# Kernel optimization log

Hardware: AMD Instinct MI355X
Metric: run time of the kernel (lower is better)

Reference implementation:

```python
import jax, jax.numpy as jnp
import numpy as np
import math

D_MODEL = 256
N_HEADS = 4
WINDOW = 5
LN_EPS = 1e-5


def setup_inputs() -> dict:
    key = jax.random.key(0)
    ks = jax.random.split(key, 10)
    B, S, D = 8, 8192, D_MODEL
    s = 1.0 / math.sqrt(D)
    x = jax.random.normal(ks[0], (B, S, D), dtype=jnp.float32)
    Wq = jax.random.uniform(ks[1], (D, D), jnp.float32, -s, s)
    bq = jax.random.uniform(ks[2], (D,), jnp.float32, -s, s)
    Wk = jax.random.uniform(ks[3], (D, D), jnp.float32, -s, s)
    bk = jax.random.uniform(ks[4], (D,), jnp.float32, -s, s)
    Wv = jax.random.uniform(ks[5], (D, D), jnp.float32, -s, s)
    bv = jax.random.uniform(ks[6], (D,), jnp.float32, -s, s)
    Wo = jax.random.uniform(ks[7], (D, D), jnp.float32, -s, s)
    bo = jax.random.uniform(ks[8], (D,), jnp.float32, -s, s)
    gamma = jnp.ones((D,), jnp.float32)
    beta = jnp.zeros((D,), jnp.float32)
    return {"x": x, "Wq": Wq, "bq": bq, "Wk": Wk, "bk": bk,
            "Wv": Wv, "bv": bv, "Wo": Wo, "bo": bo,
            "gamma": gamma, "beta": beta}


def _layer_norm(y, gamma, beta):
    mu = jnp.mean(y, axis=-1, keepdims=True)
    var = jnp.mean(jnp.square(y - mu), axis=-1, keepdims=True)
    return (y - mu) * jax.lax.rsqrt(var + LN_EPS) * gamma + beta


def reference(x, Wq, bq, Wk, bk, Wv, bv, Wo, bo, gamma, beta):
    B, S, D = x.shape
    H, hd, W = N_HEADS, D // N_HEADS, WINDOW
    num_windows = (S + W - 1) // W
    pad_len = num_windows * W - S
    Sp = S + pad_len

    def proj(Wm, bm):
        # (B,S,D) -> (B,H,S,hd)
        p = (x @ Wm.T + bm).reshape(B, S, H, hd).transpose(0, 2, 1, 3)
        if pad_len > 0:
            p = jnp.pad(p, ((0, 0), (0, 0), (0, pad_len), (0, 0)))
        return p.reshape(B, H, num_windows, W, hd)

    Q = proj(Wq, bq)
    K = proj(Wk, bk)
    V = proj(Wv, bv)

    scores = jnp.einsum('bhnwd,bhnvd->bhnwv', Q, K) / math.sqrt(hd)
    attn = jax.nn.softmax(scores, axis=-1)  # dropout is identity in eval
    out = jnp.tanh(jnp.einsum('bhnwv,bhnvd->bhnwd', attn, V))

    out = out.reshape(B, H, Sp, hd)[:, :, :S, :]
    out = out.transpose(0, 2, 1, 3).reshape(B, S, D)
    out = out @ Wo.T + bo
    return _layer_norm(out + x, gamma, beta)
```

## Files before the change

### kernel.cpp

```cpp
#include <hip/hip_runtime.h>
#include <hip/hip_bf16.h>
#include <stdint.h>

typedef unsigned short u16;
typedef __attribute__((ext_vector_type(8))) __bf16 bf16x8;
typedef __attribute__((ext_vector_type(4))) float f32x4;

#define DEV static __device__ __forceinline__

DEV u16 f32_to_bf16(float f) {
  uint32_t u = __float_as_uint(f);
  u += 0x7fffu + ((u >> 16) & 1u);
  return (u16)(u >> 16);
}

DEV void unpack8(uint4 u, float* f) {
  uint32_t a[4] = {u.x, u.y, u.z, u.w};
#pragma unroll
  for (int i = 0; i < 4; ++i) {
    f[2 * i]     = __uint_as_float(a[i] << 16);
    f[2 * i + 1] = __uint_as_float(a[i] & 0xffff0000u);
  }
}

DEV uint4 pack8(const float* f) {
  uint32_t a[4];
#pragma unroll
  for (int i = 0; i < 4; ++i)
    a[i] = (uint32_t)f32_to_bf16(f[2 * i]) | ((uint32_t)f32_to_bf16(f[2 * i + 1]) << 16);
  return make_uint4(a[0], a[1], a[2], a[3]);
}

__global__ __launch_bounds__(256) void convert_kernel(
    const float* __restrict__ x, const float* __restrict__ Wq,
    const float* __restrict__ Wk, const float* __restrict__ Wv,
    const float* __restrict__ Wo, u16* __restrict__ xb,
    u16* __restrict__ wqkv, u16* __restrict__ wob) {
  const size_t NX4 = (size_t)65536 * 256 / 4;
  size_t i = (size_t)blockIdx.x * 256 + threadIdx.x;
  const float* src;
  u16* dst;
  size_t off4;
  if (i < NX4) {
    src = x; dst = xb; off4 = i;
  } else {
    size_t w = i - NX4;
    int which = (int)(w >> 14);
    off4 = w & 16383;
    if (which == 0)      { src = Wq; dst = wqkv; }
    else if (which == 1) { src = Wk; dst = wqkv + 65536; }
    else if (which == 2) { src = Wv; dst = wqkv + 131072; }
    else                 { src = Wo; dst = wob; }
  }
  float4 v = reinterpret_cast<const float4*>(src)[off4];
  ushort4 o;
  o.x = f32_to_bf16(v.x); o.y = f32_to_bf16(v.y);
  o.z = f32_to_bf16(v.z); o.w = f32_to_bf16(v.w);
  reinterpret_cast<ushort4*>(dst)[off4] = o;
}

__global__ __launch_bounds__(256) void qkv_gemm(
    const u16* __restrict__ Xb, const u16* __restrict__ Wqkv,
    const float* __restrict__ bq, const float* __restrict__ bk,
    const float* __restrict__ bv, u16* __restrict__ QKV) {
  __shared__ u16 As[128][40];
  __shared__ u16 Bs[128][40];
  const int bn = blockIdx.x;
  const int bm = blockIdx.y;
  const int tid = threadIdx.x;
  const int lane = tid & 63;
  const int wid = tid >> 6;
  const int wm = (wid >> 1) * 64;
  const int wn = (wid & 1) * 64;
  const int fr = lane & 15;
  const int fq = lane >> 4;

  f32x4 acc[4][4] = {};

  const int tr = tid >> 1;
  const int tc = (tid & 1) << 4;
  const u16* Ag = Xb + (size_t)(bm * 128 + tr) * 256 + tc;
  const u16* Bg = Wqkv + (size_t)(bn * 128 + tr) * 256 + tc;

  for (int kt = 0; kt < 8; ++kt) {
    uint4 a0 = *reinterpret_cast<const uint4*>(Ag + kt * 32);
    uint4 a1 = *reinterpret_cast<const uint4*>(Ag + kt * 32 + 8);
    uint4 b0 = *reinterpret_cast<const uint4*>(Bg + kt * 32);
    uint4 b1 = *reinterpret_cast<const uint4*>(Bg + kt * 32 + 8);
    __syncthreads();
    *reinterpret_cast<uint4*>(&As[tr][tc]) = a0;
    *reinterpret_cast<uint4*>(&As[tr][tc + 8]) = a1;
    *reinterpret_cast<uint4*>(&Bs[tr][tc]) = b0;
    *reinterpret_cast<uint4*>(&Bs[tr][tc + 8]) = b1;
    __syncthreads();
    bf16x8 af[4], bf[4];
#pragma unroll
    for (int m = 0; m < 4; ++m)
      af[m] = *reinterpret_cast<const bf16x8*>(&As[wm + m * 16 + fr][fq * 8]);
#pragma unroll
    for (int n = 0; n < 4; ++n)
      bf[n] = *reinterpret_cast<const bf16x8*>(&Bs[wn + n * 16 + fr][fq * 8]);
#pragma unroll
    for (int m = 0; m < 4; ++m)
#pragma unroll
      for (int n = 0; n < 4; ++n)
        acc[m][n] = __builtin_amdgcn_mfma_f32_16x16x32_bf16(af[m], bf[n], acc[m][n], 0, 0, 0);
  }

  const float* bias = (bn < 2) ? (bq + (bn & 1) * 128)
                    : (bn < 4) ? (bk + ((bn - 2) & 1) * 128)
                               : (bv + ((bn - 4) & 1) * 128);
  float bv4[4];
#pragma unroll
  for (int n = 0; n < 4; ++n) bv4[n] = bias[wn + n * 16 + fr];

#pragma unroll
  for (int m = 0; m < 4; ++m) {
#pragma unroll
    for (int r = 0; r < 4; ++r) {
      int row = bm * 128 + wm + m * 16 + fq * 4 + r;
      u16* orow = QKV + (size_t)row * 768 + bn * 128;
#pragma unroll
      for (int n = 0; n < 4; ++n)
        orow[wn + n * 16 + fr] = f32_to_bf16(acc[m][n][r] + bv4[n]);
    }
  }
}

__global__ __launch_bounds__(256) void attn_kernel(const u16* __restrict__ QKV,
                                                   u16* __restrict__ AO) {
  const int S = 8192, NW = 1639, CH = 205;
  int wgid = blockIdx.x * 4 + (threadIdx.x >> 6);
  int lane = threadIdx.x & 63;
  int b = wgid / (4 * CH);
  int rm = wgid % (4 * CH);
  int h = rm / CH;
  int ch = rm % CH;
  int w = ch * 8 + (lane >> 3);
  int t = lane & 7;
  bool wv = (w < NW);

  float kv[5][8], vv[5][8];
#pragma unroll
  for (int j = 0; j < 5; ++j) {
    int s = w * 5 + j;
    if (wv && s < S) {
      size_t off = ((size_t)b * S + s) * 768 + h * 64 + t * 8;
      unpack8(*reinterpret_cast<const uint4*>(QKV + off + 256), kv[j]);
      unpack8(*reinterpret_cast<const uint4*>(QKV + off + 512), vv[j]);
    } else {
#pragma unroll
      for (int d = 0; d < 8; ++d) { kv[j][d] = 0.f; vv[j][d] = 0.f; }
    }
  }

#pragma unroll
  for (int i = 0; i < 5; ++i) {
    int s = w * 5 + i;
    bool sv = wv && (s < S);
    float q[8];
    if (sv) {
      size_t off = ((size_t)b * S + s) * 768 + h * 64 + t * 8;
      unpack8(*reinterpret_cast<const uint4*>(QKV + off), q);
    } else {
#pragma unroll
      for (int d = 0; d < 8; ++d) q[d] = 0.f;
    }
    float sc[5];
#pragma unroll
    for (int j = 0; j < 5; ++j) {
      float p = 0.f;
#pragma unroll
      for (int d = 0; d < 8; ++d) p += q[d] * kv[j][d];
      sc[j] = p;
    }
#pragma unroll
    for (int mask = 1; mask <= 4; mask <<= 1)
#pragma unroll
      for (int j = 0; j < 5; ++j) sc[j] += __shfl_xor(sc[j], mask);
#pragma unroll
    for (int j = 0; j < 5; ++j) sc[j] *= 0.125f;
    float mx = sc[0];
#pragma unroll
    for (int j = 1; j < 5; ++j) mx = fmaxf(mx, sc[j]);
    float e[5], sum = 0.f;
#pragma unroll
    for (int j = 0; j < 5; ++j) { e[j] = __expf(sc[j] - mx); sum += e[j]; }
    float inv = 1.0f / sum;
    float o[8];
#pragma unroll
    for (int d = 0; d < 8; ++d) {
      float a = 0.f;
#pragma unroll
      for (int j = 0; j < 5; ++j) a += e[j] * vv[j][d];
      float v2 = a * inv;
      float e2 = __expf(2.0f * v2);
      o[d] = 1.0f - 2.0f / (e2 + 1.0f);
    }
    if (sv) {
      size_t oo = ((size_t)b * S + s) * 256 + h * 64 + t * 8;
      *reinterpret_cast<uint4*>(AO + oo) = pack8(o);
    }
  }
}

__global__ __launch_bounds__(256) void o_gemm_ln(
    const u16* __restrict__ AO, const u16* __restrict__ Wob,
    const float* __restrict__ bo, const float* __restrict__ x,
    const float* __restrict__ gamma, const float* __restrict__ beta,
    float* __restrict__ out) {
  __shared__ u16 As[64][40];
  __shared__ u16 Bs[256][40];
  __shared__ float pS[4][64], pQ[4][64];
  __shared__ float muS[64], rsS[64];
  const int bm = blockIdx.x;
  const int tid = threadIdx.x;
  const int lane = tid & 63;
  const int wid = tid >> 6;
  const int wn = wid * 64;
  const int fr = lane & 15;
  const int fq = lane >> 4;

  f32x4 acc[4][4] = {};

  const int ar = tid >> 2;
  const int ac = (tid & 3) << 3;
  const u16* Ag = AO + (size_t)(bm * 64 + ar) * 256 + ac;

  for (int kt = 0; kt < 8; ++kt) {
    uint4 a = *reinterpret_cast<const uint4*>(Ag + kt * 32);
    uint4 bvv[4];
#pragma unroll
    for (int j = 0; j < 4; ++j)
      bvv[j] = *reinterpret_cast<const uint4*>(Wob + (size_t)(ar + j * 64) * 256 + kt * 32 + ac);
    __syncthreads();
    *reinterpret_cast<uint4*>(&As[ar][ac]) = a;
#pragma unroll
    for (int j = 0; j < 4; ++j)
      *reinterpret_cast<uint4*>(&Bs[ar + j * 64][ac]) = bvv[j];
    __syncthreads();
    bf16x8 af[4], bf[4];
#pragma unroll
    for (int m = 0; m < 4; ++m)
      af[m] = *reinterpret_cast<const bf16x8*>(&As[m * 16 + fr][fq * 8]);
#pragma unroll
    for (int n = 0; n < 4; ++n)
      bf[n] = *reinterpret_cast<const bf16x8*>(&Bs[wn + n * 16 + fr][fq * 8]);
#pragma unroll
    for (int m = 0; m < 4; ++m)
#pragma unroll
      for (int n = 0; n < 4; ++n)
        acc[m][n] = __builtin_amdgcn_mfma_f32_16x16x32_bf16(af[m], bf[n], acc[m][n], 0, 0, 0);
  }

  float bov[4], gv[4], bev[4];
#pragma unroll
  for (int n = 0; n < 4; ++n) {
    int c = wn + n * 16 + fr;
    bov[n] = bo[c]; gv[n] = gamma[c]; bev[n] = beta[c];
  }
#pragma unroll
  for (int m = 0; m < 4; ++m)
#pragma unroll
    for (int r = 0; r < 4; ++r) {
      size_t rg = (size_t)(bm * 64 + m * 16 + fq * 4 + r);
#pragma unroll
      for (int n = 0; n < 4; ++n)
        acc[m][n][r] += bov[n] + x[rg * 256 + wn + n * 16 + fr];
    }

#pragma unroll
  for (int m = 0; m < 4; ++m)
#pragma unroll
    for (int r = 0; r < 4; ++r) {
      float s1 = 0.f, s2 = 0.f;
#pragma unroll
      for (int n = 0; n < 4; ++n) {
        float vx = acc[m][n][r];
        s1 += vx; s2 += vx * vx;
      }
#pragma unroll
      for (int mask = 1; mask <= 8; mask <<= 1) {
        s1 += __shfl_xor(s1, mask);
        s2 += __shfl_xor(s2, mask);
      }
      if (fr == 0) {
        int row = m * 16 + fq * 4 + r;
        pS[wid][row] = s1; pQ[wid][row] = s2;
      }
    }
  __syncthreads();
  if (tid < 64) {
    float s1 = pS[0][tid] + pS[1][tid] + pS[2][tid] + pS[3][tid];
    float s2 = pQ[0][tid] + pQ[1][tid] + pQ[2][tid] + pQ[3][tid];
    float mu = s1 * (1.0f / 256.0f);
    float var = s2 * (1.0f / 256.0f) - mu * mu;
    muS[tid] = mu;
    rsS[tid] = rsqrtf(var + 1e-5f);
  }
  __syncthreads();
#pragma unroll
  for (int m = 0; m < 4; ++m)
#pragma unroll
    for (int r = 0; r < 4; ++r) {
      int row = m * 16 + fq * 4 + r;
      float mu = muS[row], rs = rsS[row];
      float* orow = out + (size_t)(bm * 64 + row) * 256;
#pragma unroll
      for (int n = 0; n < 4; ++n)
        orow[wn + n * 16 + fr] = (acc[m][n][r] - mu) * rs * gv[n] + bev[n];
    }
}

extern "C" void kernel_launch(void* const* d_in, const int* in_sizes, int n_in,
                              void* d_out, int out_size, void* d_ws, size_t ws_size,
                              hipStream_t stream) {
  const float* x     = (const float*)d_in[0];
  const float* Wq    = (const float*)d_in[1];
  const float* bq    = (const float*)d_in[2];
  const float* Wk    = (const float*)d_in[3];
  const float* bk    = (const float*)d_in[4];
  const float* Wv    = (const float*)d_in[5];
  const float* bv    = (const float*)d_in[6];
  const float* Wo    = (const float*)d_in[7];
  const float* bo    = (const float*)d_in[8];
  const float* gamma = (const float*)d_in[9];
  const float* beta  = (const float*)d_in[10];
  float* out = (float*)d_out;

  char* ws = (char*)d_ws;
  u16* xb   = (u16*)(ws);
  u16* wqkv = (u16*)(ws + 33554432);
  u16* wob  = (u16*)(ws + 33947648);
  u16* qkv  = (u16*)(ws + 34078720);
  u16* ao   = (u16*)(ws + 134742016);

  convert_kernel<<<16640, 256, 0, stream>>>(x, Wq, Wk, Wv, Wo, xb, wqkv, wob);
  dim3 g1(6, 512);
  qkv_gemm<<<g1, 256, 0, stream>>>(xb, wqkv, bq, bk, bv, qkv);
  attn_kernel<<<1640, 256, 0, stream>>>(qkv, ao);
  o_gemm_ln<<<1024, 256, 0, stream>>>(ao, wob, bo, x, gamma, beta, out);
}
```

Baseline: 286.0 us.

## Fuse x bf16 conversion into QKV GEMM and drop LDS staging in GEMMs

Removes the separate pass that converts the full activation x to bf16; the QKV GEMM now reads fp32 x directly and converts fragments in registers, saving a 32MB write and reread. Both GEMMs drop shared-memory tiling and __syncthreads, loading MFMA fragments straight from global memory, with smaller 32-row tiles and more blocks. The cost is that tiles are reused less: operand reuse now depends on the cache rather than LDS, and the A fragments are read redundantly by each of the four waves.

```diff
diff --git a/kernel.cpp b/kernel.cpp
--- a/kernel.cpp
+++ b/kernel.cpp
@@ -31,27 +31,27 @@
   return make_uint4(a[0], a[1], a[2], a[3]);
 }
 
-__global__ __launch_bounds__(256) void convert_kernel(
-    const float* __restrict__ x, const float* __restrict__ Wq,
-    const float* __restrict__ Wk, const float* __restrict__ Wv,
-    const float* __restrict__ Wo, u16* __restrict__ xb,
+DEV bf16x8 cvt8(float4 a, float4 b) {
+  union { u16 h[8]; bf16x8 v; } u;
+  u.h[0] = f32_to_bf16(a.x); u.h[1] = f32_to_bf16(a.y);
+  u.h[2] = f32_to_bf16(a.z); u.h[3] = f32_to_bf16(a.w);
+  u.h[4] = f32_to_bf16(b.x); u.h[5] = f32_to_bf16(b.y);
+  u.h[6] = f32_to_bf16(b.z); u.h[7] = f32_to_bf16(b.w);
+  return u.v;
+}
+
+__global__ __launch_bounds__(256) void convert_w(
+    const float* __restrict__ Wq, const float* __restrict__ Wk,
+    const float* __restrict__ Wv, const float* __restrict__ Wo,
     u16* __restrict__ wqkv, u16* __restrict__ wob) {
-  const size_t NX4 = (size_t)65536 * 256 / 4;
-  size_t i = (size_t)blockIdx.x * 256 + threadIdx.x;
-  const float* src;
-  u16* dst;
-  size_t off4;
-  if (i < NX4) {
-    src = x; dst = xb; off4 = i;
-  } else {
-    size_t w = i - NX4;
-    int which = (int)(w >> 14);
-    off4 = w & 16383;
-    if (which == 0)      { src = Wq; dst = wqkv; }
-    else if (which == 1) { src = Wk; dst = wqkv + 65536; }
-    else if (which == 2) { src = Wv; dst = wqkv + 131072; }
-    else                 { src = Wo; dst = wob; }
-  }
+  int i = blockIdx.x * 256 + threadIdx.x;
+  int which = i >> 14;
+  int off4 = i & 16383;
+  const float* src; u16* dst;
+  if (which == 0)      { src = Wq; dst = wqkv; }
+  else if (which == 1) { src = Wk; dst = wqkv + 65536; }
+  else if (which == 2) { src = Wv; dst = wqkv + 131072; }
+  else                 { src = Wo; dst = wob; }
   float4 v = reinterpret_cast<const float4*>(src)[off4];
   ushort4 o;
   o.x = f32_to_bf16(v.x); o.y = f32_to_bf16(v.y);
@@ -59,72 +59,58 @@
   reinterpret_cast<ushort4*>(dst)[off4] = o;
 }
 
-__global__ __launch_bounds__(256) void qkv_gemm(
-    const u16* __restrict__ Xb, const u16* __restrict__ Wqkv,
+__global__ __launch_bounds__(256) void qkv_gemm2(
+    const float* __restrict__ x, const u16* __restrict__ Wqkv,
     const float* __restrict__ bq, const float* __restrict__ bk,
     const float* __restrict__ bv, u16* __restrict__ QKV) {
-  __shared__ u16 As[128][40];
-  __shared__ u16 Bs[128][40];
   const int bn = blockIdx.x;
   const int bm = blockIdx.y;
-  const int tid = threadIdx.x;
-  const int lane = tid & 63;
-  const int wid = tid >> 6;
-  const int wm = (wid >> 1) * 64;
-  const int wn = (wid & 1) * 64;
+  const int lane = threadIdx.x & 63;
+  const int wid = threadIdx.x >> 6;
   const int fr = lane & 15;
   const int fq = lane >> 4;
-
-  f32x4 acc[4][4] = {};
-
-  const int tr = tid >> 1;
-  const int tc = (tid & 1) << 4;
-  const u16* Ag = Xb + (size_t)(bm * 128 + tr) * 256 + tc;
-  const u16* Bg = Wqkv + (size_t)(bn * 128 + tr) * 256 + tc;
+  const int row0 = bm * 32;
+  const int colw = wid * 64;
+
+  const float* Ag = x + (size_t)(row0 + fr) * 256 + fq * 8;
+  const u16* Bg = Wqkv + ((size_t)bn * 256 + colw + fr) * 256 + fq * 8;
+
+  f32x4 acc[2][4] = {};
 
   for (int kt = 0; kt < 8; ++kt) {
-    uint4 a0 = *reinterpret_cast<const uint4*>(Ag + kt * 32);
-    uint4 a1 = *reinterpret_cast<const uint4*>(Ag + kt * 32 + 8);
-    uint4 b0 = *reinterpret_cast<const uint4*>(Bg + kt * 32);
-    uint4 b1 = *reinterpret_cast<const uint4*>(Bg + kt * 32 + 8);
-    __syncthreads();
-    *reinterpret_cast<uint4*>(&As[tr][tc]) = a0;
-    *reinterpret_cast<uint4*>(&As[tr][tc + 8]) = a1;
-    *reinterpret_cast<uint4*>(&Bs[tr][tc]) = b0;
-    *reinterpret_cast<uint4*>(&Bs[tr][tc + 8]) = b1;
-    __syncthreads();
-    bf16x8 af[4], bf[4];
-#pragma unroll
-    for (int m = 0; m < 4; ++m)
-      af[m] = *reinterpret_cast<const bf16x8*>(&As[wm + m * 16 + fr][fq * 8]);
+    bf16x8 af[2], bf[4];
+#pragma unroll
+    for (int m = 0; m < 2; ++m) {
+      const float* p = Ag + (size_t)(m * 16) * 256 + kt * 32;
+      float4 u0 = *reinterpret_cast<const float4*>(p);
+      float4 u1 = *reinterpret_cast<const float4*>(p + 4);
+      af[m] = cvt8(u0, u1);
+    }
 #pragma unroll
     for (int n = 0; n < 4; ++n)
-      bf[n] = *reinterpret_cast<const bf16x8*>(&Bs[wn + n * 16 + fr][fq * 8]);
-#pragma unroll
-    for (int m = 0; m < 4; ++m)
+      bf[n] = *reinterpret_cast<const bf16x8*>(Bg + (size_t)(n * 16) * 256 + kt * 32);
+#pragma unroll
+    for (int m = 0; m < 2; ++m)
 #pragma unroll
       for (int n = 0; n < 4; ++n)
         acc[m][n] = __builtin_amdgcn_mfma_f32_16x16x32_bf16(af[m], bf[n], acc[m][n], 0, 0, 0);
   }
 
-  const float* bias = (bn < 2) ? (bq + (bn & 1) * 128)
-                    : (bn < 4) ? (bk + ((bn - 2) & 1) * 128)
-                               : (bv + ((bn - 4) & 1) * 128);
+  const float* bias = (bn == 0) ? bq : (bn == 1) ? bk : bv;
   float bv4[4];
 #pragma unroll
-  for (int n = 0; n < 4; ++n) bv4[n] = bias[wn + n * 16 + fr];
-
-#pragma unroll
-  for (int m = 0; m < 4; ++m) {
+  for (int n = 0; n < 4; ++n) bv4[n] = bias[colw + n * 16 + fr];
+
+#pragma unroll
+  for (int m = 0; m < 2; ++m)
 #pragma unroll
     for (int r = 0; r < 4; ++r) {
-      int row = bm * 128 + wm + m * 16 + fq * 4 + r;
-      u16* orow = QKV + (size_t)row * 768 + bn * 128;
-#pragma unroll
-      for (int n = 0; n < 4; ++n)
-        orow[wn + n * 16 + fr] = f32_to_bf16(acc[m][n][r] + bv4[n]);
-    }
-  }
+      int row = row0 + m * 16 + fq * 4 + r;
+      u16* orow = QKV + (size_t)row * 768 + bn * 256 + colw;
+#pragma unroll
+      for (int n = 0; n < 4; ++n)
+        orow[n * 16 + fr] = f32_to_bf16(acc[m][n][r] + bv4[n]);
+    }
 }
 
 __global__ __launch_bounds__(256) void attn_kernel(const u16* __restrict__ QKV,
@@ -204,50 +190,36 @@
   }
 }
 
-__global__ __launch_bounds__(256) void o_gemm_ln(
+__global__ __launch_bounds__(256) void o_gemm_ln2(
     const u16* __restrict__ AO, const u16* __restrict__ Wob,
     const float* __restrict__ bo, const float* __restrict__ x,
     const float* __restrict__ gamma, const float* __restrict__ beta,
     float* __restrict__ out) {
-  __shared__ u16 As[64][40];
-  __shared__ u16 Bs[256][40];
-  __shared__ float pS[4][64], pQ[4][64];
-  __shared__ float muS[64], rsS[64];
+  __shared__ float pS[4][32], pQ[4][32], muS[32], rsS[32];
   const int bm = blockIdx.x;
   const int tid = threadIdx.x;
   const int lane = tid & 63;
   const int wid = tid >> 6;
-  const int wn = wid * 64;
   const int fr = lane & 15;
   const int fq = lane >> 4;
-
-  f32x4 acc[4][4] = {};
-
-  const int ar = tid >> 2;
-  const int ac = (tid & 3) << 3;
-  const u16* Ag = AO + (size_t)(bm * 64 + ar) * 256 + ac;
+  const int row0 = bm * 32;
+  const int col0 = wid * 64;
+
+  const u16* Ag = AO + (size_t)(row0 + fr) * 256 + fq * 8;
+  const u16* Bg = Wob + (size_t)(col0 + fr) * 256 + fq * 8;
+
+  f32x4 acc[2][4] = {};
 
   for (int kt = 0; kt < 8; ++kt) {
-    uint4 a = *reinterpret_cast<const uint4*>(Ag + kt * 32);
-    uint4 bvv[4];
-#pragma unroll
-    for (int j = 0; j < 4; ++j)
-      bvv[j] = *reinterpret_cast<const uint4*>(Wob + (size_t)(ar + j * 64) * 256 + kt * 32 + ac);
-    __syncthreads();
-    *reinterpret_cast<uint4*>(&As[ar][ac]) = a;
-#pragma unroll
-    for (int j = 0; j < 4; ++j)
-      *reinterpret_cast<uint4*>(&Bs[ar + j * 64][ac]) = bvv[j];
-    __syncthreads();
-    bf16x8 af[4], bf[4];
-#pragma unroll
-    for (int m = 0; m < 4; ++m)
-      af[m] = *reinterpret_cast<const bf16x8*>(&As[m * 16 + fr][fq * 8]);
+    bf16x8 af[2], bf[4];
+#pragma unroll
+    for (int m = 0; m < 2; ++m)
+      af[m] = *reinterpret_cast<const bf16x8*>(Ag + (size_t)(m * 16) * 256 + kt * 32);
 #pragma unroll
     for (int n = 0; n < 4; ++n)
-      bf[n] = *reinterpret_cast<const bf16x8*>(&Bs[wn + n * 16 + fr][fq * 8]);
-#pragma unroll
-    for (int m = 0; m < 4; ++m)
+      bf[n] = *reinterpret_cast<const bf16x8*>(Bg + (size_t)(n * 16) * 256 + kt * 32);
+#pragma unroll
+    for (int m = 0; m < 2; ++m)
 #pragma unroll
       for (int n = 0; n < 4; ++n)
         acc[m][n] = __builtin_amdgcn_mfma_f32_16x16x32_bf16(af[m], bf[n], acc[m][n], 0, 0, 0);
@@ -256,21 +228,21 @@
   float bov[4], gv[4], bev[4];
 #pragma unroll
   for (int n = 0; n < 4; ++n) {
-    int c = wn + n * 16 + fr;
+    int c = col0 + n * 16 + fr;
     bov[n] = bo[c]; gv[n] = gamma[c]; bev[n] = beta[c];
   }
 #pragma unroll
-  for (int m = 0; m < 4; ++m)
+  for (int m = 0; m < 2; ++m)
 #pragma unroll
     for (int r = 0; r < 4; ++r) {
-      size_t rg = (size_t)(bm * 64 + m * 16 + fq * 4 + r);
-#pragma unroll
-      for (int n = 0; n < 4; ++n)
-        acc[m][n][r] += bov[n] + x[rg * 256 + wn + n * 16 + fr];
-    }
-
-#pragma unroll
-  for (int m = 0; m < 4; ++m)
+      size_t rg = (size_t)(row0 + m * 16 + fq * 4 + r);
+#pragma unroll
+      for (int n = 0; n < 4; ++n)
+        acc[m][n][r] += bov[n] + x[rg * 256 + col0 + n * 16 + fr];
+    }
+
+#pragma unroll
+  for (int m = 0; m < 2; ++m)
 #pragma unroll
     for (int r = 0; r < 4; ++r) {
       float s1 = 0.f, s2 = 0.f;
@@ -290,7 +262,7 @@
       }
     }
   __syncthreads();
-  if (tid < 64) {
+  if (tid < 32) {
     float s1 = pS[0][tid] + pS[1][tid] + pS[2][tid] + pS[3][tid];
     float s2 = pQ[0][tid] + pQ[1][tid] + pQ[2][tid] + pQ[3][tid];
     float mu = s1 * (1.0f / 256.0f);
@@ -300,15 +272,15 @@
   }
   __syncthreads();
 #pragma unroll
-  for (int m = 0; m < 4; ++m)
+  for (int m = 0; m < 2; ++m)
 #pragma unroll
     for (int r = 0; r < 4; ++r) {
       int row = m * 16 + fq * 4 + r;
       float mu = muS[row], rs = rsS[row];
-      float* orow = out + (size_t)(bm * 64 + row) * 256;
-#pragma unroll
-      for (int n = 0; n < 4; ++n)
-        orow[wn + n * 16 + fr] = (acc[m][n][r] - mu) * rs * gv[n] + bev[n];
+      float* orow = out + (size_t)(row0 + row) * 256;
+#pragma unroll
+      for (int n = 0; n < 4; ++n)
+        orow[col0 + n * 16 + fr] = (acc[m][n][r] - mu) * rs * gv[n] + bev[n];
     }
 }
 
@@ -329,15 +301,14 @@
   float* out = (float*)d_out;
 
   char* ws = (char*)d_ws;
-  u16* xb   = (u16*)(ws);
-  u16* wqkv = (u16*)(ws + 33554432);
-  u16* wob  = (u16*)(ws + 33947648);
-  u16* qkv  = (u16*)(ws + 34078720);
-  u16* ao   = (u16*)(ws + 134742016);
-
-  convert_kernel<<<16640, 256, 0, stream>>>(x, Wq, Wk, Wv, Wo, xb, wqkv, wob);
-  dim3 g1(6, 512);
-  qkv_gemm<<<g1, 256, 0, stream>>>(xb, wqkv, bq, bk, bv, qkv);
+  u16* wqkv = (u16*)(ws);
+  u16* wob  = (u16*)(ws + 393216);
+  u16* qkv  = (u16*)(ws + 524288);
+  u16* ao   = (u16*)(ws + 101187584);
+
+  convert_w<<<256, 256, 0, stream>>>(Wq, Wk, Wv, Wo, wqkv, wob);
+  dim3 g1(3, 2048);
+  qkv_gemm2<<<g1, 256, 0, stream>>>(x, wqkv, bq, bk, bv, qkv);
   attn_kernel<<<1640, 256, 0, stream>>>(qkv, ao);
-  o_gemm_ln<<<1024, 256, 0, stream>>>(ao, wob, bo, x, gamma, beta, out);
-}
+  o_gemm_ln2<<<2048, 256, 0, stream>>>(ao, wob, bo, x, gamma, beta, out);
+}
```

After: 378.8 us. +32.4%, slower.

## Load GEMM tiles directly into LDS with XOR swizzle and block remap

Applied to the files above, without the earlier changes.

Both GEMM kernels now stage their A/B tiles with global_load_lds, which writes directly to shared memory without passing through registers. The padded LDS tiles are replaced by unpadded tiles that use an XOR swizzle to avoid bank conflicts. The QKV GEMM also gets a 1D grid with a block-index swizzle to improve L2 locality, and a trailing barrier is added per k-step. The intent is to cut register staging and VGPR use. The loop is still single-buffered with two barriers per iteration, so load latency is not overlapped.

```diff
diff --git a/kernel.cpp b/kernel.cpp
--- a/kernel.cpp
+++ b/kernel.cpp
@@ -29,6 +29,12 @@
   for (int i = 0; i < 4; ++i)
     a[i] = (uint32_t)f32_to_bf16(f[2 * i]) | ((uint32_t)f32_to_bf16(f[2 * i + 1]) << 16);
   return make_uint4(a[0], a[1], a[2], a[3]);
+}
+
+DEV void gload16(const u16* g, u16* l) {
+  __builtin_amdgcn_global_load_lds(
+      (const __attribute__((address_space(1))) void*)g,
+      (__attribute__((address_space(3))) void*)l, 16, 0, 0);
 }
 
 __global__ __launch_bounds__(256) void convert_kernel(
@@ -59,14 +65,16 @@
   reinterpret_cast<ushort4*>(dst)[off4] = o;
 }
 
-__global__ __launch_bounds__(256) void qkv_gemm(
+__global__ __launch_bounds__(256) void qkv_gemm3(
     const u16* __restrict__ Xb, const u16* __restrict__ Wqkv,
     const float* __restrict__ bq, const float* __restrict__ bk,
     const float* __restrict__ bv, u16* __restrict__ QKV) {
-  __shared__ u16 As[128][40];
-  __shared__ u16 Bs[128][40];
-  const int bn = blockIdx.x;
-  const int bm = blockIdx.y;
+  __shared__ __align__(16) u16 As[128 * 32];
+  __shared__ __align__(16) u16 Bs[128 * 32];
+  const int bid = blockIdx.x;
+  const int swz = (bid & 7) * 384 + (bid >> 3);
+  const int bn = swz % 6;
+  const int bm = swz / 6;
   const int tid = threadIdx.x;
   const int lane = tid & 63;
   const int wid = tid >> 6;
@@ -75,36 +83,43 @@
   const int fr = lane & 15;
   const int fq = lane >> 4;
 
+  const int c0 = tid, c1 = tid + 256;
+  const int r0c = c0 >> 2, s0 = (c0 ^ (c0 >> 2)) & 3;
+  const int r1c = c1 >> 2, s1 = (c1 ^ (c1 >> 2)) & 3;
+  const u16* Ag0 = Xb + (size_t)(bm * 128 + r0c) * 256 + s0 * 8;
+  const u16* Ag1 = Xb + (size_t)(bm * 128 + r1c) * 256 + s1 * 8;
+  const u16* Bg0 = Wqkv + (size_t)(bn * 128 + r0c) * 256 + s0 * 8;
+  const u16* Bg1 = Wqkv + (size_t)(bn * 128 + r1c) * 256 + s1 * 8;
+  u16* lA0 = As + c0 * 8;
+  u16* lA1 = As + c1 * 8;
+  u16* lB0 = Bs + c0 * 8;
+  u16* lB1 = Bs + c1 * 8;
+
   f32x4 acc[4][4] = {};
 
-  const int tr = tid >> 1;
-  const int tc = (tid & 1) << 4;
-  const u16* Ag = Xb + (size_t)(bm * 128 + tr) * 256 + tc;
-  const u16* Bg = Wqkv + (size_t)(bn * 128 + tr) * 256 + tc;
-
   for (int kt = 0; kt < 8; ++kt) {
-    uint4 a0 = *reinterpret_cast<const uint4*>(Ag + kt * 32);
-    uint4 a1 = *reinterpret_cast<const uint4*>(Ag + kt * 32 + 8);
-    uint4 b0 = *reinterpret_cast<const uint4*>(Bg + kt * 32);
-    uint4 b1 = *reinterpret_cast<const uint4*>(Bg + kt * 32 + 8);
-    __syncthreads();
-    *reinterpret_cast<uint4*>(&As[tr][tc]) = a0;
-    *reinterpret_cast<uint4*>(&As[tr][tc + 8]) = a1;
-    *reinterpret_cast<uint4*>(&Bs[tr][tc]) = b0;
-    *reinterpret_cast<uint4*>(&Bs[tr][tc + 8]) = b1;
+    gload16(Ag0 + kt * 32, lA0);
+    gload16(Ag1 + kt * 32, lA1);
+    gload16(Bg0 + kt * 32, lB0);
+    gload16(Bg1 + kt * 32, lB1);
     __syncthreads();
     bf16x8 af[4], bf[4];
 #pragma unroll
+    for (int m = 0; m < 4; ++m) {
+      int row = wm + m * 16 + fr;
+      af[m] = *reinterpret_cast<const bf16x8*>(As + row * 32 + ((fq ^ (row & 3)) * 8));
+    }
+#pragma unroll
+    for (int n = 0; n < 4; ++n) {
+      int row = wn + n * 16 + fr;
+      bf[n] = *reinterpret_cast<const bf16x8*>(Bs + row * 32 + ((fq ^ (row & 3)) * 8));
+    }
+#pragma unroll
     for (int m = 0; m < 4; ++m)
-      af[m] = *reinterpret_cast<const bf16x8*>(&As[wm + m * 16 + fr][fq * 8]);
-#pragma unroll
-    for (int n = 0; n < 4; ++n)
-      bf[n] = *reinterpret_cast<const bf16x8*>(&Bs[wn + n * 16 + fr][fq * 8]);
-#pragma unroll
-    for (int m = 0; m < 4; ++m)
 #pragma unroll
       for (int n = 0; n < 4; ++n)
         acc[m][n] = __builtin_amdgcn_mfma_f32_16x16x32_bf16(af[m], bf[n], acc[m][n], 0, 0, 0);
+    __syncthreads();
   }
 
   const float* bias = (bn < 2) ? (bq + (bn & 1) * 128)
@@ -115,7 +130,7 @@
   for (int n = 0; n < 4; ++n) bv4[n] = bias[wn + n * 16 + fr];
 
 #pragma unroll
-  for (int m = 0; m < 4; ++m) {
+  for (int m = 0; m < 4; ++m)
 #pragma unroll
     for (int r = 0; r < 4; ++r) {
       int row = bm * 128 + wm + m * 16 + fq * 4 + r;
@@ -124,7 +139,6 @@
       for (int n = 0; n < 4; ++n)
         orow[wn + n * 16 + fr] = f32_to_bf16(acc[m][n][r] + bv4[n]);
     }
-  }
 }
 
 __global__ __launch_bounds__(256) void attn_kernel(const u16* __restrict__ QKV,
@@ -204,15 +218,14 @@
   }
 }
 
-__global__ __launch_bounds__(256) void o_gemm_ln(
+__global__ __launch_bounds__(256) void o_gemm_ln3(
     const u16* __restrict__ AO, const u16* __restrict__ Wob,
     const float* __restrict__ bo, const float* __restrict__ x,
     const float* __restrict__ gamma, const float* __restrict__ beta,
     float* __restrict__ out) {
-  __shared__ u16 As[64][40];
-  __shared__ u16 Bs[256][40];
-  __shared__ float pS[4][64], pQ[4][64];
-  __shared__ float muS[64], rsS[64];
+  __shared__ __align__(16) u16 As[64 * 32];
+  __shared__ __align__(16) u16 Bs[256 * 32];
+  __shared__ float pS[4][64], pQ[4][64], muS[64], rsS[64];
   const int bm = blockIdx.x;
   const int tid = threadIdx.x;
   const int lane = tid & 63;
@@ -220,37 +233,46 @@
   const int wn = wid * 64;
   const int fr = lane & 15;
   const int fq = lane >> 4;
+  const int row0 = bm * 64;
+
+  const int ra = tid >> 2, sa = (tid ^ (tid >> 2)) & 3;
+  const u16* Ag = AO + (size_t)(row0 + ra) * 256 + sa * 8;
+  u16* lA = As + tid * 8;
+  const u16* Bg0 = Wob + (size_t)((tid) >> 2) * 256 + (((tid) ^ ((tid) >> 2)) & 3) * 8;
+  const u16* Bg1 = Wob + (size_t)((tid + 256) >> 2) * 256 + (((tid + 256) ^ ((tid + 256) >> 2)) & 3) * 8;
+  const u16* Bg2 = Wob + (size_t)((tid + 512) >> 2) * 256 + (((tid + 512) ^ ((tid + 512) >> 2)) & 3) * 8;
+  const u16* Bg3 = Wob + (size_t)((tid + 768) >> 2) * 256 + (((tid + 768) ^ ((tid + 768) >> 2)) & 3) * 8;
+  u16* lB0 = Bs + tid * 8;
+  u16* lB1 = Bs + (tid + 256) * 8;
+  u16* lB2 = Bs + (tid + 512) * 8;
+  u16* lB3 = Bs + (tid + 768) * 8;
 
   f32x4 acc[4][4] = {};
 
-  const int ar = tid >> 2;
-  const int ac = (tid & 3) << 3;
-  const u16* Ag = AO + (size_t)(bm * 64 + ar) * 256 + ac;
-
   for (int kt = 0; kt < 8; ++kt) {
-    uint4 a = *reinterpret_cast<const uint4*>(Ag + kt * 32);
-    uint4 bvv[4];
-#pragma unroll
-    for (int j = 0; j < 4; ++j)
-      bvv[j] = *reinterpret_cast<const uint4*>(Wob + (size_t)(ar + j * 64) * 256 + kt * 32 + ac);
-    __syncthreads();
-    *reinterpret_cast<uint4*>(&As[ar][ac]) = a;
-#pragma unroll
-    for (int j = 0; j < 4; ++j)
-      *reinterpret_cast<uint4*>(&Bs[ar + j * 64][ac]) = bvv[j];
+    gload16(Ag + kt * 32, lA);
+    gload16(Bg0 + kt * 32, lB0);
+    gload16(Bg1 + kt * 32, lB1);
+    gload16(Bg2 + kt * 32, lB2);
+    gload16(Bg3 + kt * 32, lB3);
     __syncthreads();
     bf16x8 af[4], bf[4];
 #pragma unroll
+    for (int m = 0; m < 4; ++m) {
+      int row = m * 16 + fr;
+      af[m] = *reinterpret_cast<const bf16x8*>(As + row * 32 + ((fq ^ (row & 3)) * 8));
+    }
+#pragma unroll
+    for (int n = 0; n < 4; ++n) {
+      int row = wn + n * 16 + fr;
+      bf[n] = *reinterpret_cast<const bf16x8*>(Bs + row * 32 + ((fq ^ (row & 3)) * 8));
+    }
+#pragma unroll
     for (int m = 0; m < 4; ++m)
-      af[m] = *reinterpret_cast<const bf16x8*>(&As[m * 16 + fr][fq * 8]);
-#pragma unroll
-    for (int n = 0; n < 4; ++n)
-      bf[n] = *reinterpret_cast<const bf16x8*>(&Bs[wn + n * 16 + fr][fq * 8]);
-#pragma unroll
-    for (int m = 0; m < 4; ++m)
 #pragma unroll
       for (int n = 0; n < 4; ++n)
         acc[m][n] = __builtin_amdgcn_mfma_f32_16x16x32_bf16(af[m], bf[n], acc[m][n], 0, 0, 0);
+    __syncthreads();
   }
 
   float bov[4], gv[4], bev[4];
@@ -263,7 +285,7 @@
   for (int m = 0; m < 4; ++m)
 #pragma unroll
     for (int r = 0; r < 4; ++r) {
-      size_t rg = (size_t)(bm * 64 + m * 16 + fq * 4 + r);
+      size_t rg = (size_t)(row0 + m * 16 + fq * 4 + r);
 #pragma unroll
       for (int n = 0; n < 4; ++n)
         acc[m][n][r] += bov[n] + x[rg * 256 + wn + n * 16 + fr];
@@ -305,7 +327,7 @@
     for (int r = 0; r < 4; ++r) {
       int row = m * 16 + fq * 4 + r;
       float mu = muS[row], rs = rsS[row];
-      float* orow = out + (size_t)(bm * 64 + row) * 256;
+      float* orow = out + (size_t)(row0 + row) * 256;
 #pragma unroll
       for (int n = 0; n < 4; ++n)
         orow[wn + n * 16 + fr] = (acc[m][n][r] - mu) * rs * gv[n] + bev[n];
@@ -336,8 +358,7 @@
   u16* ao   = (u16*)(ws + 134742016);
 
   convert_kernel<<<16640, 256, 0, stream>>>(x, Wq, Wk, Wv, Wo, xb, wqkv, wob);
-  dim3 g1(6, 512);
-  qkv_gemm<<<g1, 256, 0, stream>>>(xb, wqkv, bq, bk, bv, qkv);
+  qkv_gemm3<<<3072, 256, 0, stream>>>(xb, wqkv, bq, bk, bv, qkv);
   attn_kernel<<<1640, 256, 0, stream>>>(qkv, ao);
-  o_gemm_ln<<<1024, 256, 0, stream>>>(ao, wob, bo, x, gamma, beta, out);
-}
+  o_gemm_ln3<<<1024, 256, 0, stream>>>(ao, wob, bo, x, gamma, beta, out);
+}
```

Result: faster. 236.8 us (-17.2%).
